# Optimization experiments

Hardware: AMD Instinct MI355X
Metric: run time of the kernel (lower is better)

Reference implementation:

```python
import jax, jax.numpy as jnp
import numpy as np

N, E, D, H, DK, T, R, KN, KR = 50000, 800000, 128, 8, 16, 3, 4, 2, 2

def setup_inputs() -> dict:
    key = jax.random.key(0)
    ks = jax.random.split(key, 16)
    lin_s = np.sqrt(1.0 / D).astype(np.float32)   # ~ nn.Linear init scale
    glo_s = np.sqrt(2.0 / (DK + DK)).astype(np.float32)  # glorot for [*,H,DK,DK]
    return {
        'x': jax.random.normal(ks[0], (N, D), jnp.float32),
        'Wk': jax.random.normal(ks[1], (KN, D, D), jnp.float32) * lin_s,
        'bk': jnp.zeros((KN, D), jnp.float32),
        'Wq': jax.random.normal(ks[2], (KN, D, D), jnp.float32) * lin_s,
        'bq': jnp.zeros((KN, D), jnp.float32),
        'Wv': jax.random.normal(ks[3], (KN, D, D), jnp.float32) * lin_s,
        'bv': jnp.zeros((KN, D), jnp.float32),
        'rel_pri': jnp.ones((KR, H), jnp.float32),
        'rel_att': jax.random.normal(ks[4], (KR, H, DK, DK), jnp.float32) * glo_s,
        'rel_msg': jax.random.normal(ks[5], (KR, H, DK, DK), jnp.float32) * glo_s,
        'n_alpha': jax.random.normal(ks[6], (T, KN), jnp.float32) * 0.001,
        'r_alpha': jax.random.normal(ks[7], (R, KR), jnp.float32) * 0.001,
        'W_up': jax.random.normal(ks[8], (T, D, D), jnp.float32) * lin_s,
        'b_up': jnp.zeros((T, D), jnp.float32),
        'gamma': jnp.ones((T, D), jnp.float32),
        'beta': jnp.zeros((T, D), jnp.float32),
        'edge_index': jax.random.randint(ks[9], (2, E), 0, N),
        'node_type': jax.random.randint(ks[10], (N,), 0, T),
        'edge_type': jax.random.randint(ks[11], (E,), 0, R),
    }

def reference(x, Wk, bk, Wq, bq, Wv, bv, rel_pri, rel_att, rel_msg,
              n_alpha, r_alpha, W_up, b_up, gamma, beta,
              edge_index, node_type, edge_type):
    n, d = x.shape
    h = rel_att.shape[1]; dk = d // h
    n_types = W_up.shape[0]; n_rel = r_alpha.shape[0]
    # NAS-mixed per-node-type k/q/v linears
    an = jax.nn.softmax(n_alpha, axis=-1)[node_type]        # [N, KN]
    def mix(W, b):
        cand = jnp.einsum('nd,kdo->kno', x, W) + b[:, None, :]  # [KN, N, D]
        return jnp.einsum('kno,nk->no', cand, an).reshape(n, h, dk)
    k = mix(Wk, bk); q = mix(Wq, bq); v = mix(Wv, bv)
    # NAS-mixed per-relation bilinear att/msg and priority
    br = jax.nn.softmax(r_alpha, axis=-1)                   # [R, KR]
    att_r = jnp.einsum('rk,khde->rhde', br, rel_att)        # [R, H, DK, DK]
    msg_r = jnp.einsum('rk,khde->rhde', br, rel_msg)
    pri_r = br @ rel_pri                                    # [R, H]
    src, dst = edge_index[0], edge_index[1]
    k_e = k[src]; q_e = q[dst]; v_e = v[src]                # [E, H, DK]
    k_t = jnp.zeros_like(k_e); m_t = jnp.zeros_like(v_e)
    for r in range(n_rel):  # small fixed relation loop
        sel = (edge_type == r)[:, None, None]
        k_t = k_t + jnp.where(sel, jnp.einsum('ehd,hdo->eho', k_e, att_r[r]), 0.0)
        m_t = m_t + jnp.where(sel, jnp.einsum('ehd,hdo->eho', v_e, msg_r[r]), 0.0)
    score = (q_e * k_t).sum(-1) * pri_r[edge_type] / np.float32(np.sqrt(dk))  # [E, H]
    # segment softmax over destination nodes
    mx = jax.ops.segment_max(score, dst, num_segments=n)
    ex = jnp.exp(score - mx[dst])
    den = jax.ops.segment_sum(ex, dst, num_segments=n)
    w = ex / (den[dst] + 1e-16)                             # [E, H]
    out = jax.ops.segment_sum(m_t * w[..., None], dst, num_segments=n).reshape(n, d)
    # heterogeneous update: gelu -> per-type linear -> residual -> per-type LN
    res = jax.nn.gelu(out)
    trans = jnp.zeros_like(x)
    for t in range(n_types):
        sel = (node_type == t)[:, None]
        trans = trans + jnp.where(sel, res @ W_up[t] + b_up[t], 0.0)
    hres = trans + x
    mu = hres.mean(-1, keepdims=True)
    var = hres.var(-1, keepdims=True)
    hn = (hres - mu) / jnp.sqrt(var + 1e-5)
    return hn * gamma[node_type] + beta[node_type]
```

## Files before the change

### kernel.cpp

```cpp
#include <hip/hip_runtime.h>
#include <hip/hip_bf16.h>

#define DEV __device__ __forceinline__

using frag8 = __attribute__((ext_vector_type(8))) short;
using f32x4 = __attribute__((ext_vector_type(4))) float;

DEV float b2f(__hip_bfloat16 v){ return __bfloat162float(v); }
DEV __hip_bfloat16 f2b(float f){ return __float2bfloat16(f); }
DEV short f2s(float f){ __hip_bfloat16 h = __float2bfloat16(f); short s; __builtin_memcpy(&s,&h,2); return s; }
DEV float bflo(unsigned u){ unsigned x = u<<16; float f; __builtin_memcpy(&f,&x,4); return f; }
DEV float bfhi(unsigned u){ unsigned x = u&0xFFFF0000u; float f; __builtin_memcpy(&f,&x,4); return f; }
DEV unsigned packbf(float a, float b){
  return (unsigned)(unsigned short)f2s(a) | ((unsigned)(unsigned short)f2s(b)<<16);
}

DEV bool is_bf16_mode(const void* rel_pri){
  return ((const unsigned*)rel_pri)[0] == 0x3F803F80u;
}
DEV float ldf(const void* p, int i, bool isbf){
  return isbf ? __bfloat162float(((const __hip_bfloat16*)p)[i]) : ((const float*)p)[i];
}

#if __has_builtin(__builtin_amdgcn_fdot2_f32_bf16)
typedef __bf16 bf16x2 __attribute__((ext_vector_type(2)));
DEV float dot2b(unsigned a, unsigned b, float c){
  bf16x2 av, bv; __builtin_memcpy(&av,&a,4); __builtin_memcpy(&bv,&b,4);
  return __builtin_amdgcn_fdot2_f32_bf16(av, bv, c, false);
}
#else
DEV float dot2b(unsigned a, unsigned b, float c){
  return c + bflo(a)*bflo(b) + bfhi(a)*bfhi(b);
}
#endif

DEV float gelu_f(float v){
  float z2 = v*(1.5957691216057308f + 0.07135481627f*v*v);
  return v/(1.f + __expf(-z2));
}

struct PrepArgs {
  const void *x,*Wk,*Wq,*Wv,*bk,*bq,*bv,*rel_pri,*rel_att,*rel_msg,*n_alpha,*r_alpha,*Wup,*bup,*gm,*bt;
  const int* ntype;
  float *anW,*priS,*bmixK,*bqt,*bvm,*upc;
  __hip_bfloat16 *bsw,*wsw,*msw2,*xb;
  int* count3;
  int N;
};

__global__ void k_prep(PrepArgs P){
  bool isbf = is_bf16_mode(P.rel_pri);
  float an[3][2], br[4][2];
  #pragma unroll
  for (int t=0;t<3;t++){
    float a0=ldf(P.n_alpha,t*2,isbf), a1=ldf(P.n_alpha,t*2+1,isbf);
    float m=fmaxf(a0,a1); float e0=__expf(a0-m), e1=__expf(a1-m); float inv=1.f/(e0+e1);
    an[t][0]=e0*inv; an[t][1]=e1*inv;
  }
  #pragma unroll
  for (int r=0;r<4;r++){
    float a0=ldf(P.r_alpha,r*2,isbf), a1=ldf(P.r_alpha,r*2+1,isbf);
    float m=fmaxf(a0,a1); float e0=__expf(a0-m), e1=__expf(a1-m); float inv=1.f/(e0+e1);
    br[r][0]=e0*inv; br[r][1]=e1*inv;
  }
  int g = blockIdx.x*blockDim.x + threadIdx.x;
  int stride = gridDim.x*blockDim.x;

  if (!isbf){
    const float4* xf = (const float4*)P.x;
    for (int idx=g; idx<P.N*16; idx+=stride){
      float4 u = xf[(size_t)idx*2], v = xf[(size_t)idx*2+1];
      frag8 r;
      r[0]=f2s(u.x); r[1]=f2s(u.y); r[2]=f2s(u.z); r[3]=f2s(u.w);
      r[4]=f2s(v.x); r[5]=f2s(v.y); r[6]=f2s(v.z); r[7]=f2s(v.w);
      *reinterpret_cast<frag8*>(P.xb + (size_t)idx*8) = r;
    }
  }

  for (int idx=g; idx<196608; idx+=stride){
    int jj = idx&7, lane=(idx>>3)&63, s=(idx>>9)&3, tile=(idx>>11)&15, chunk=idx>>15;
    int k = s*32 + ((lane>>4)<<3) + jj;
    int col = tile*16 + (lane&15);
    int cand = col>>7, c = col&127;
    float v;
    if (chunk==0)      v = ldf(P.Wk, cand*16384 + k*128 + c, isbf);
    else if (chunk==1) v = ldf(P.Wv, cand*16384 + k*128 + c, isbf);
    else {
      int r = chunk-2, h = c>>4, d = c&15;
      float acc=0.f;
      #pragma unroll
      for (int o=0;o<16;o++){
        float att = br[r][0]*ldf(P.rel_att,(h*16+d)*16+o,isbf) + br[r][1]*ldf(P.rel_att,2048+(h*16+d)*16+o,isbf);
        acc += ldf(P.Wq, cand*16384 + k*128 + h*16+o, isbf) * att;
      }
      v = acc;
    }
    P.bsw[idx] = f2b(v);
  }
  for (int idx=g; idx<49152; idx+=stride){
    int t3 = idx>>14, f = idx&16383;
    int jj=f&7, lane=(f>>3)&63, s=(f>>9)&3, nt=f>>11;
    int k = s*32 + ((lane>>4)<<3)+jj;
    int cc = nt*16 + (lane&15);
    P.wsw[idx] = f2b(ldf(P.Wup, t3*16384 + k*128 + cc, isbf));
  }
  for (int idx=g; idx<65536; idx+=stride){
    int rel = idx>>14, f = idx&16383;
    int jj=f&7, lane=(f>>3)&63, s=(f>>9)&3, tile=(f>>11)&7;
    int k = s*32 + ((lane>>4)<<3)+jj;
    int col = tile*16 + (lane&15);
    int h = k>>4, d = k&15;
    int h2 = col>>4, o = col&15;
    float v = 0.f;
    if (h2==h)
      v = br[rel][0]*ldf(P.rel_msg,(h*16+d)*16+o,isbf) + br[rel][1]*ldf(P.rel_msg,2048+(h*16+d)*16+o,isbf);
    P.msw2[idx] = f2b(v);
  }
  for (int idx=g; idx<384; idx+=stride){
    int t = idx>>7, c = idx&127;
    P.bmixK[idx] = an[t][0]*ldf(P.bk,c,isbf) + an[t][1]*ldf(P.bk,128+c,isbf);
  }
  for (int idx=g; idx<1536; idx+=stride){
    int t = idx>>9, rem = idx&511, r = rem>>7, c = rem&127;
    int h = c>>4, d = c&15;
    float acc=0.f;
    #pragma unroll
    for (int o=0;o<16;o++){
      float att = br[r][0]*ldf(P.rel_att,(h*16+d)*16+o,isbf) + br[r][1]*ldf(P.rel_att,2048+(h*16+d)*16+o,isbf);
      float bqm = an[t][0]*ldf(P.bq,h*16+o,isbf) + an[t][1]*ldf(P.bq,128+h*16+o,isbf);
      acc += bqm*att;
    }
    P.bqt[idx] = acc;
  }
  for (int idx=g; idx<384; idx+=stride){
    int t = idx>>7, c = idx&127;
    P.bvm[idx] = an[t][0]*ldf(P.bv,c,isbf) + an[t][1]*ldf(P.bv,128+c,isbf);
  }
  for (int idx=g; idx<1152; idx+=stride){
    int p = idx/384, rem = idx - p*384;
    const void* src = p==0 ? P.bup : p==1 ? P.gm : P.bt;
    P.upc[idx] = ldf(src, rem, isbf);
  }
  for (int idx=g; idx<32; idx+=stride){
    int r = idx>>3, h = idx&7;
    P.priS[idx] = 0.25f*(br[r][0]*ldf(P.rel_pri,h,isbf) + br[r][1]*ldf(P.rel_pri,8+h,isbf));
  }
  for (int idx=g; idx<6; idx+=stride) P.anW[idx] = an[idx>>1][idx&1];
  {
    int c0=0, c1=0, c2=0;
    for (int idx=g; idx<P.N; idx+=stride){
      int t = P.ntype[idx];
      c0 += (t==0); c1 += (t==1); c2 += (t==2);
    }
    #pragma unroll
    for (int m=1; m<64; m<<=1){
      c0 += __shfl_xor(c0, m, 64);
      c1 += __shfl_xor(c1, m, 64);
      c2 += __shfl_xor(c2, m, 64);
    }
    if ((threadIdx.x & 63) == 0){
      if (c0) atomicAdd(&P.count3[0], c0);
      if (c1) atomicAdd(&P.count3[1], c1);
      if (c2) atomicAdd(&P.count3[2], c2);
    }
  }
}

__global__ void k_hist(const int* __restrict__ eidx, int* __restrict__ count, int E){
  int e = blockIdx.x*256 + threadIdx.x;
  if (e < E) atomicAdd(&count[eidx[E+e]], 1);
}

__global__ __launch_bounds__(1024) void k_scan1(const int* __restrict__ count, int* __restrict__ excl,
                                                int* __restrict__ ctot, int N){
  __shared__ int s[1024];
  int i = blockIdx.x*1024 + threadIdx.x;
  int v = (i < N) ? count[i] : 0;
  s[threadIdx.x] = v;
  __syncthreads();
  int run = v;
  for (int off=1; off<1024; off<<=1){
    int add = (threadIdx.x >= off) ? s[threadIdx.x - off] : 0;
    __syncthreads();
    run += add; s[threadIdx.x] = run;
    __syncthreads();
  }
  if (i < N) excl[i] = run - v;
  if (threadIdx.x == 1023) ctot[blockIdx.x] = run;
}

__global__ void k_scan2(const int* __restrict__ ctot, int* __restrict__ coff,
                        const int* __restrict__ c3, int* __restrict__ segp, int NC){
  if (threadIdx.x==0 && blockIdx.x==0){
    int run=0;
    for (int c=0;c<NC;c++){ coff[c]=run; run+=ctot[c]; }
    int a0 = (c3[0]+127)&~127;
    int a1 = (c3[1]+127)&~127;
    int a2 = (c3[2]+127)&~127;
    segp[0]=0; segp[1]=a0; segp[2]=a0+a1; segp[3]=a0+a1+a2;
  }
}

__global__ __launch_bounds__(256) void k_nscatter(const int* __restrict__ ntype, const int* __restrict__ segp,
                           int* __restrict__ cur3, int* __restrict__ nlist, int N){
  __shared__ int wcnt[4][3];
  __shared__ int tbase[3];
  int tid = threadIdx.x;
  int n = blockIdx.x*256 + tid;
  int w = tid>>6, lane = tid&63;
  int t = (n < N) ? ntype[n] : -1;
  unsigned long long b0 = __ballot(t==0);
  unsigned long long b1 = __ballot(t==1);
  unsigned long long b2 = __ballot(t==2);
  if (lane==0){
    wcnt[w][0] = __popcll(b0);
    wcnt[w][1] = __popcll(b1);
    wcnt[w][2] = __popcll(b2);
  }
  __syncthreads();
  if (tid < 3){
    int c = wcnt[0][tid]+wcnt[1][tid]+wcnt[2][tid]+wcnt[3][tid];
    tbase[tid] = c ? atomicAdd(&cur3[tid], c) : 0;
  }
  __syncthreads();
  if (t >= 0){
    unsigned long long mask = t==0?b0 : t==1?b1 : b2;
    int lanerank = __popcll(mask & ((1ULL<<lane)-1ULL));
    int waveoff = 0;
    #pragma unroll
    for (int ww=0; ww<4; ww++) if (ww < w) waveoff += wcnt[ww][t];
    nlist[segp[t] + tbase[t] + waveoff + lanerank] = n;
  }
}

__global__ void k_escatter(const int* __restrict__ eidx, const int* __restrict__ etype,
                           const int* __restrict__ coff, const int* __restrict__ excl,
                           int* __restrict__ cursor, int* __restrict__ pack, int E){
  int e = blockIdx.x*256 + threadIdx.x;
  if (e < E){
    int src = eidx[e];
    int dst = eidx[E+e];
    int rt  = etype[e];
    int pos = coff[dst>>10] + excl[dst] + atomicAdd(&cursor[dst], 1);
    pack[pos] = src | (rt<<20);
  }
}

__global__ __launch_bounds__(256) void k_qkvqt(
    const void* __restrict__ x, const __hip_bfloat16* __restrict__ xb,
    const int* __restrict__ ntype,
    const void* __restrict__ relp,
    const __hip_bfloat16* __restrict__ bsw, const float* __restrict__ anW,
    const float* __restrict__ bmixK, const float* __restrict__ bmixV,
    const float* __restrict__ bqt,
    __hip_bfloat16* __restrict__ kb, __hip_bfloat16* __restrict__ vb,
    __hip_bfloat16* __restrict__ qtb, int N, int perx)
{
  __shared__ __hip_bfloat16 Bs[16384];
  __shared__ __align__(16) __hip_bfloat16 Os[128*72];
  bool isbf = is_bf16_mode(relp);
  int tid = threadIdx.x;
  int w = tid>>6, lane = tid&63;
  int m16 = lane&15, q4 = lane>>4;

  int nrb = (N+127)>>7;
  int xcd  = blockIdx.x & 7;
  int slot = blockIdx.x >> 3;
  int lrb  = slot/12;
  int sub  = slot - lrb*12;
  int rb   = xcd*perx + lrb;
  if (rb >= nrb) return;
  int chunk = sub >> 1;
  int hh    = sub & 1;
  int base  = rb*128;

  const int4* bsw4 = reinterpret_cast<const int4*>(bsw) + chunk*4096;
  int4* Bs4 = reinterpret_cast<int4*>(Bs);
  #pragma unroll
  for (int u=0;u<8;u++){
    int srcT = 4*hh + (u&3) + ((u>>2)<<3);
    __builtin_amdgcn_global_load_lds(
        (const __attribute__((address_space(1))) void*)(bsw4 + srcT*256 + tid),
        (__attribute__((address_space(3))) void*)(Bs4 + u*256 + tid),
        16, 0, 0);
  }

  const __hip_bfloat16* xs = isbf ? (const __hip_bfloat16*)x : xb;
  frag8 a0[4], a1[4];
  {
    int rr0 = base + w*32 + m16;
    int rr1 = rr0 + 16;
    int r0 = rr0 < N ? rr0 : N-1;
    int r1 = rr1 < N ? rr1 : N-1;
    #pragma unroll
    for (int s=0;s<4;s++){
      a0[s] = *reinterpret_cast<const frag8*>(xs + (size_t)r0*128 + q4*8 + s*32);
      a1[s] = *reinterpret_cast<const frag8*>(xs + (size_t)r1*128 + q4*8 + s*32);
    }
  }
  float e0[8], e1[8]; int tt8[8];
  #pragma unroll
  for (int u=0;u<8;u++){
    int rs = u>>2, i = u&3;
    int rr = base + w*32 + rs*16 + q4*4 + i;
    int rc = rr < N ? rr : N-1;
    int t = ntype[rc]; tt8[u] = t;
    e0[u] = anW[t*2]; e1[u] = anW[t*2+1];
  }
  float b0p[4], b1p[4], b2p[4];
  #pragma unroll
  for (int p=0;p<4;p++){
    int c = (4*hh + p)*16 + m16;
    if (chunk < 2){
      const float* bb = (chunk==0) ? bmixK : bmixV;
      b0p[p] = bb[c]; b1p[p] = bb[128+c]; b2p[p] = bb[256+c];
    } else {
      int r = chunk-2;
      b0p[p] = bqt[(0*4+r)*128 + c];
      b1p[p] = bqt[(1*4+r)*128 + c];
      b2p[p] = bqt[(2*4+r)*128 + c];
    }
  }
  __syncthreads();
  const frag8* Bf = reinterpret_cast<const frag8*>(Bs);
  #pragma unroll
  for (int p=0;p<4;p++){
    f32x4 c00={0,0,0,0}, c01={0,0,0,0}, c10={0,0,0,0}, c11={0,0,0,0};
    #pragma unroll
    for (int s=0;s<4;s++){
      frag8 b0 = Bf[(p*4+s)*64 + lane];
      frag8 b1 = Bf[((p+4)*4+s)*64 + lane];
      c00 = __builtin_amdgcn_mfma_f32_16x16x32_bf16(a0[s], b0, c00, 0,0,0);
      c01 = __builtin_amdgcn_mfma_f32_16x16x32_bf16(a1[s], b0, c01, 0,0,0);
      c10 = __builtin_amdgcn_mfma_f32_16x16x32_bf16(a0[s], b1, c10, 0,0,0);
      c11 = __builtin_amdgcn_mfma_f32_16x16x32_bf16(a1[s], b1, c11, 0,0,0);
    }
    int cl = p*16 + m16;
    #pragma unroll
    for (int u=0;u<8;u++){
      int rs = u>>2, i = u&3;
      float v0 = rs ? c01[i] : c00[i];
      float v1 = rs ? c11[i] : c10[i];
      int t = tt8[u];
      float bs = (t==0) ? b0p[p] : (t==1) ? b1p[p] : b2p[p];
      float val = e0[u]*v0 + e1[u]*v1 + bs;
      int rl = w*32 + rs*16 + q4*4 + i;
      Os[rl*72 + cl] = f2b(val);
    }
  }
  __syncthreads();
  #pragma unroll
  for (int it=0; it<4; it++){
    int idx = it*256 + tid;
    int rl = idx>>3, sl = idx&7;
    int row = base + rl;
    if (row < N){
      int4 val = *reinterpret_cast<const int4*>(
          reinterpret_cast<const char*>(Os) + rl*144 + sl*16);
      if (chunk < 2)
        *reinterpret_cast<int4*>((chunk==0?kb:vb) + (size_t)row*128 + hh*64 + sl*8) = val;
      else
        *reinterpret_cast<int4*>(qtb + (size_t)row*512 + (chunk-2)*128 + hh*64 + sl*8) = val;
    }
  }
}

__global__ __launch_bounds__(256) void k_vmsg(
    const __hip_bfloat16* __restrict__ vb,
    const __hip_bfloat16* __restrict__ msw2,
    __hip_bfloat16* __restrict__ vmb, int N, int perx)
{
  __shared__ __hip_bfloat16 Bs[16384];
  __shared__ __align__(16) __hip_bfloat16 Os[128*72];
  int tid = threadIdx.x, w = tid>>6, lane = tid&63, m16 = lane&15, q4 = lane>>4;
  int nrb = (N+127)>>7;
  int xcd = blockIdx.x & 7, slot = blockIdx.x>>3;
  int lrb = slot>>3, sub = slot&7;
  int rel = sub>>1, hh = sub&1;
  int rb = xcd*perx + lrb;
  if (rb >= nrb) return;
  int base = rb*128;

  const int4* m4 = reinterpret_cast<const int4*>(msw2) + rel*2048;
  int4* Bs4 = reinterpret_cast<int4*>(Bs);
  #pragma unroll
  for (int u=0;u<4;u++)
    __builtin_amdgcn_global_load_lds(
        (const __attribute__((address_space(1))) void*)(m4 + (4*hh+u)*256 + tid),
        (__attribute__((address_space(3))) void*)(Bs4 + u*256 + tid), 16, 0, 0);

  frag8 a0[4], a1[4];
  int rr0 = base + w*32 + m16, rr1 = rr0+16;
  int r0 = rr0<N?rr0:N-1, r1 = rr1<N?rr1:N-1;
  #pragma unroll
  for (int s=0;s<4;s++){
    a0[s] = *reinterpret_cast<const frag8*>(vb + (size_t)r0*128 + q4*8 + s*32);
    a1[s] = *reinterpret_cast<const frag8*>(vb + (size_t)r1*128 + q4*8 + s*32);
  }
  __syncthreads();
  const frag8* Bf = reinterpret_cast<const frag8*>(Bs);
  #pragma unroll
  for (int p=0;p<4;p++){
    f32x4 c0={0,0,0,0}, c1={0,0,0,0};
    #pragma unroll
    for (int s=0;s<4;s++){
      frag8 b = Bf[(p*4+s)*64 + lane];
      c0 = __builtin_amdgcn_mfma_f32_16x16x32_bf16(a0[s], b, c0, 0,0,0);
      c1 = __builtin_amdgcn_mfma_f32_16x16x32_bf16(a1[s], b, c1, 0,0,0);
    }
    int cl = p*16 + m16;
    #pragma unroll
    for (int u=0;u<8;u++){
      int rs = u>>2, i = u&3;
      float v = rs ? c1[i] : c0[i];
      int rl = w*32 + rs*16 + q4*4 + i;
      Os[rl*72 + cl] = f2b(v);
    }
  }
  __syncthreads();
  #pragma unroll
  for (int it=0; it<4; it++){
    int idx = it*256 + tid;
    int rl = idx>>3, sl = idx&7;
    int row = base + rl;
    if (row < N){
      int4 val = *reinterpret_cast<const int4*>(
          reinterpret_cast<const char*>(Os) + rl*144 + sl*16);
      *reinterpret_cast<int4*>(vmb + (size_t)row*512 + rel*128 + hh*64 + sl*8) = val;
    }
  }
}

__global__ __launch_bounds__(256) void k_aggr(
  const __hip_bfloat16* __restrict__ kb, const __hip_bfloat16* __restrict__ vmb,
  const __hip_bfloat16* __restrict__ qtb,
  const int* __restrict__ count, const int* __restrict__ excl, const int* __restrict__ coff,
  const int* __restrict__ pack, const float* __restrict__ priS,
  __hip_bfloat16* __restrict__ accb, float* __restrict__ denb, int N)
{
  __shared__ int4 Qs[4][64];
  int w = threadIdx.x>>6, lane = threadIdx.x&63;
  int n = blockIdx.x*4 + w; if (n >= N) return;
  int sub = lane&15, e4 = lane>>4;
  int h = sub>>1, half = sub&1;
  const char* kbB = (const char*)kb;
  const char* vmB = (const char*)vmb;
  int start = coff[n>>10] + excl[n];
  int deg = count[n];

  Qs[w][lane] = ((const int4*)qtb)[(size_t)n*64 + lane];
  float ps0 = priS[h], ps1 = priS[8+h], ps2 = priS[16+h], ps3 = priS[24+h];
  unsigned sub16 = (unsigned)sub<<4;

  float acc[8];
  #pragma unroll
  for (int d=0;d<8;d++) acc[d]=0.f;
  float den = 0.f;

  for (int b0=0; b0<deg; b0+=64){
    int m = deg - b0; if (m > 64) m = 64;
    int pk = (lane < m) ? pack[start + b0 + lane] : 0;
    int nst = (m + 3)>>2;
    int4 K={0,0,0,0}, V={0,0,0,0}; int RT=0; bool A=false;
    auto issue = [&](int st){
      int j = st*4 + e4;
      A = j < m;
      int pe = __shfl(pk, j, 64);
      RT = (pe>>20)&3;
      unsigned src = (unsigned)(pe & 0xFFFFF);
      if (A){
        K = *(const int4*)(kbB + ((src<<8) + sub16));
        V = *(const int4*)(vmB + ((src<<10) + ((unsigned)RT<<8) + sub16));
      } else {
        K = int4{0,0,0,0}; V = int4{0,0,0,0};
      }
    };
    issue(0);
    for (int st=0; st<nst; st++){
      int4 kc=K, vc=V; int rt=RT; bool a=A;
      if (st+1 < nst) issue(st+1);
      int4 qc = Qs[w][rt*16 + sub];
      float psr = rt==0 ? ps0 : rt==1 ? ps1 : rt==2 ? ps2 : ps3;
      float s = dot2b((unsigned)kc.x,(unsigned)qc.x,0.f);
      s = dot2b((unsigned)kc.y,(unsigned)qc.y,s);
      s = dot2b((unsigned)kc.z,(unsigned)qc.z,s);
      s = dot2b((unsigned)kc.w,(unsigned)qc.w,s);
      s += __shfl_xor(s, 1, 64);
      float ex = a ? __expf(fminf(s*psr, 30.f)) : 0.f;
      den += half ? 0.f : ex;
      unsigned vv[4]={(unsigned)vc.x,(unsigned)vc.y,(unsigned)vc.z,(unsigned)vc.w};
      #pragma unroll
      for (int q=0;q<4;q++){
        acc[2*q]   += ex*bflo(vv[q]);
        acc[2*q+1] += ex*bfhi(vv[q]);
      }
    }
  }
  #pragma unroll
  for (int m2=16; m2<64; m2<<=1){
    #pragma unroll
    for (int d=0;d<8;d++) acc[d] += __shfl_xor(acc[d], m2, 64);
    den += __shfl_xor(den, m2, 64);
  }
  if (e4==0){
    unsigned o0 = packbf(acc[0], acc[1]);
    unsigned o1 = packbf(acc[2], acc[3]);
    unsigned o2 = packbf(acc[4], acc[5]);
    unsigned o3 = packbf(acc[6], acc[7]);
    int4 o4; o4.x=(int)o0; o4.y=(int)o1; o4.z=(int)o2; o4.w=(int)o3;
    ((int4*)accb)[(size_t)n*16 + sub] = o4;
    if (half==0) denb[(size_t)n*8 + h] = den;
  }
}

__global__ __launch_bounds__(256) void k_msgup(
  const __hip_bfloat16* __restrict__ accb, const float* __restrict__ denb,
  const void* __restrict__ x, const void* __restrict__ relp,
  const int* __restrict__ nlist, const int* __restrict__ segp,
  const __hip_bfloat16* __restrict__ wsw,
  const float* __restrict__ upc, void* __restrict__ out, int N)
{
  __shared__ __hip_bfloat16 Ms[16384];
  __shared__ __hip_bfloat16 resS[64*136];
  __shared__ int nrow[64];
  bool isbf = is_bf16_mode(relp);
  int tid=threadIdx.x, w=tid>>6, lane=tid&63, m16=lane&15, q4=lane>>4;
  int pos0 = blockIdx.x*64;
  int sg1 = segp[1], sg2 = segp[2];
  int t = (pos0 >= sg2) ? 2 : (pos0 >= sg1) ? 1 : 0;
  if (tid < 64) nrow[tid] = nlist[pos0 + tid];
  const int4* wsw4 = reinterpret_cast<const int4*>(wsw) + t*2048;
  int4* Ms4 = reinterpret_cast<int4*>(Ms);
  #pragma unroll
  for (int u=0;u<8;u++)
    __builtin_amdgcn_global_load_lds(
        (const __attribute__((address_space(1))) void*)(wsw4 + u*256 + tid),
        (__attribute__((address_space(3))) void*)(Ms4 + u*256 + tid), 16, 0, 0);
  __syncthreads();

  int nC[4]; float xr[4][8];
  #pragma unroll
  for (int u=0;u<4;u++){
    int rr = w*16 + q4*4 + u;
    int nid = nrow[rr]; nC[u] = nid;
    int nc = nid<0?0:nid;
    #pragma unroll
    for (int nt=0;nt<8;nt++){
      int col = nt*16+m16;
      xr[u][nt] = isbf ? b2f(((const __hip_bfloat16*)x)[(size_t)nc*128+col])
                       : ((const float*)x)[(size_t)nc*128+col];
    }
  }

  const int4* acc4 = (const int4*)accb;
  #pragma unroll
  for (int it=0; it<4; it++){
    int t2 = it*256 + tid;
    int row = t2>>4, seg = t2&15;
    int nid = nrow[row]; int nc = nid<0?0:nid;
    int4 a = acc4[(size_t)nc*16 + seg];
    float rdn = 1.f/(denb[(size_t)nc*8 + (seg>>1)] + 1e-16f);
    unsigned uu[4] = {(unsigned)a.x,(unsigned)a.y,(unsigned)a.z,(unsigned)a.w};
    unsigned ov[4];
    #pragma unroll
    for (int q=0;q<4;q++){
      float v0 = bflo(uu[q])*rdn, v1 = bfhi(uu[q])*rdn;
      ov[q] = packbf(gelu_f(v0), gelu_f(v1));
    }
    int4 o4; o4.x=(int)ov[0]; o4.y=(int)ov[1]; o4.z=(int)ov[2]; o4.w=(int)ov[3];
    *reinterpret_cast<int4*>(reinterpret_cast<char*>(resS) + row*272 + seg*16) = o4;
  }
  __syncthreads();

  f32x4 d[8];
  #pragma unroll
  for (int nt=0;nt<8;nt++) d[nt]={0,0,0,0};
  const frag8* Bf2 = reinterpret_cast<const frag8*>(Ms);
  #pragma unroll
  for (int s=0;s<4;s++){
    frag8 a = *reinterpret_cast<const frag8*>(&resS[(w*16 + m16)*136 + s*32 + q4*8]);
    #pragma unroll
    for (int nt=0;nt<8;nt++){
      frag8 b = Bf2[(nt*4+s)*64 + lane];
      d[nt] = __builtin_amdgcn_mfma_f32_16x16x32_bf16(a, b, d[nt], 0,0,0);
    }
  }
  #pragma unroll
  for (int u=0;u<4;u++){
    int nid = nC[u];
    float hv[8], s1=0.f, s2=0.f;
    #pragma unroll
    for (int nt=0;nt<8;nt++){
      int col = nt*16+m16;
      float v = d[nt][u] + upc[t*128+col] + xr[u][nt];
      hv[nt]=v; s1+=v; s2+=v*v;
    }
    #pragma unroll
    for (int mm=1; mm<16; mm<<=1){ s1 += __shfl_xor(s1, mm, 16); s2 += __shfl_xor(s2, mm, 16); }
    float mu = s1*(1.f/128.f);
    float var = s2*(1.f/128.f) - mu*mu;
    float rcp = rsqrtf(var + 1e-5f);
    if (nid >= 0){
      #pragma unroll
      for (int nt=0;nt<8;nt++){
        int col = nt*16+m16;
        float o = (hv[nt]-mu)*rcp*upc[384 + t*128+col] + upc[768 + t*128+col];
        if (isbf) ((__hip_bfloat16*)out)[(size_t)nid*128+col] = f2b(o);
        else      ((float*)out)[(size_t)nid*128+col] = o;
      }
    }
  }
}

extern "C" void kernel_launch(void* const* d_in, const int* in_sizes, int n_in,
                              void* d_out, int out_size, void* d_ws, size_t ws_size,
                              hipStream_t stream)
{
  const int* eidx  = (const int*)d_in[16];
  const int* ntype = (const int*)d_in[17];
  const int* etype = (const int*)d_in[18];

  const int N  = in_sizes[0]/128;
  const int E  = in_sizes[18];
  const int NC = (N + 1023)/1024;

  char* ws = (char*)d_ws;
  size_t off = 0;
  auto alloc = [&](size_t bytes){ size_t o = off; off += (bytes + 255) & ~(size_t)255; return o; };
  size_t o_count = alloc((size_t)N*4);
  size_t o_cursor= alloc((size_t)N*4);
  size_t o_c3    = alloc(16);
  size_t o_cur3  = alloc(16);
  size_t zbytes  = off;
  size_t o_nlist = alloc((size_t)(N+1024)*4);
  size_t o_excl  = alloc((size_t)N*4);
  size_t o_ctot  = alloc(256);
  size_t o_coff  = alloc(256);
  size_t o_segp  = alloc(16);
  size_t o_an    = alloc(6*4);
  size_t o_pri   = alloc(32*4);
  size_t o_bmk   = alloc(384*4);
  size_t o_bmv   = alloc(384*4);
  size_t o_bqt   = alloc(1536*4);
  size_t o_upc   = alloc(1152*4);
  size_t o_bsw   = alloc(196608*2);
  size_t o_wsw   = alloc(49152*2);
  size_t o_msw   = alloc(65536*2);
  size_t o_pack  = alloc((size_t)E*4);
  size_t o_xb    = alloc((size_t)N*128*2);
  size_t o_kb    = alloc((size_t)N*128*2);
  size_t o_vb    = alloc((size_t)N*128*2);
  size_t o_qt    = alloc((size_t)N*512*2);
  size_t o_vm    = alloc((size_t)N*512*2);
  size_t o_acc   = alloc((size_t)N*128*2);
  size_t o_den   = alloc((size_t)N*8*4);
  (void)ws_size; (void)n_in; (void)out_size;

  hipMemsetAsync(ws, 0, zbytes, stream);
  hipMemsetAsync(ws + o_nlist, 0xFF, (size_t)(N+1024)*4, stream);

  PrepArgs P;
  P.x=d_in[0];
  P.Wk=d_in[1]; P.bk=d_in[2]; P.Wq=d_in[3]; P.bq=d_in[4]; P.Wv=d_in[5]; P.bv=d_in[6];
  P.rel_pri=d_in[7]; P.rel_att=d_in[8]; P.rel_msg=d_in[9];
  P.n_alpha=d_in[10]; P.r_alpha=d_in[11]; P.Wup=d_in[12]; P.bup=d_in[13]; P.gm=d_in[14]; P.bt=d_in[15];
  P.ntype=ntype;
  P.anW=(float*)(ws+o_an); P.priS=(float*)(ws+o_pri);
  P.bmixK=(float*)(ws+o_bmk); P.bqt=(float*)(ws+o_bqt); P.bvm=(float*)(ws+o_bmv);
  P.upc=(float*)(ws+o_upc);
  P.bsw=(__hip_bfloat16*)(ws+o_bsw); P.wsw=(__hip_bfloat16*)(ws+o_wsw);
  P.msw2=(__hip_bfloat16*)(ws+o_msw);
  P.xb=(__hip_bfloat16*)(ws+o_xb);
  P.count3=(int*)(ws+o_c3); P.N=N;
  k_prep<<<1024, 256, 0, stream>>>(P);

  k_hist<<<(E+255)/256, 256, 0, stream>>>(eidx, (int*)(ws+o_count), E);
  k_scan1<<<NC, 1024, 0, stream>>>((const int*)(ws+o_count), (int*)(ws+o_excl), (int*)(ws+o_ctot), N);
  k_scan2<<<1, 64, 0, stream>>>((const int*)(ws+o_ctot), (int*)(ws+o_coff),
                                (const int*)(ws+o_c3), (int*)(ws+o_segp), NC);
  k_nscatter<<<(N+255)/256, 256, 0, stream>>>(ntype, (const int*)(ws+o_segp),
                                              (int*)(ws+o_cur3), (int*)(ws+o_nlist), N);
  k_escatter<<<(E+255)/256, 256, 0, stream>>>(eidx, etype, (const int*)(ws+o_coff),
                                              (const int*)(ws+o_excl), (int*)(ws+o_cursor),
                                              (int*)(ws+o_pack), E);
  int nrb  = (N + 127)/128;
  int perx = (nrb + 7)/8;
  k_qkvqt<<<perx*12*8, 256, 0, stream>>>(d_in[0], (const __hip_bfloat16*)(ws+o_xb), ntype, d_in[7],
                                           (const __hip_bfloat16*)(ws+o_bsw),
                                           (const float*)(ws+o_an), (const float*)(ws+o_bmk),
                                           (const float*)(ws+o_bmv),
                                           (const float*)(ws+o_bqt),
                                           (__hip_bfloat16*)(ws+o_kb), (__hip_bfloat16*)(ws+o_vb),
                                           (__hip_bfloat16*)(ws+o_qt), N, perx);
  k_vmsg<<<perx*8*8, 256, 0, stream>>>((const __hip_bfloat16*)(ws+o_vb),
                                       (const __hip_bfloat16*)(ws+o_msw),
                                       (__hip_bfloat16*)(ws+o_vm), N, perx);
  k_aggr<<<(N+3)/4, 256, 0, stream>>>((const __hip_bfloat16*)(ws+o_kb), (const __hip_bfloat16*)(ws+o_vm),
                                (const __hip_bfloat16*)(ws+o_qt),
                                (const int*)(ws+o_count), (const int*)(ws+o_excl),
                                (const int*)(ws+o_coff), (const int*)(ws+o_pack),
                                (const float*)(ws+o_pri),
                                (__hip_bfloat16*)(ws+o_acc), (float*)(ws+o_den), N);
  int gUp = (N + 444)/64;
  k_msgup<<<gUp, 256, 0, stream>>>((const __hip_bfloat16*)(ws+o_acc), (const float*)(ws+o_den),
                                   d_in[0], d_in[7],
                                   (const int*)(ws+o_nlist), (const int*)(ws+o_segp),
                                   (const __hip_bfloat16*)(ws+o_wsw),
                                   (const float*)(ws+o_upc), d_out, N);
}
```

Measured before the change: 397.2 us.

## Apply relation message transform after aggregation instead of precomputing per-relation V

Removes the k_vmsg kernel that materialized V·msg for all four relations per node. The aggregation kernel now gathers raw V and keeps four per-relation accumulators, writing a 4x wider acc buffer. The msg matrices are then applied once per destination node by an MFMA in k_msgup, before normalization and GELU. This trades a large intermediate write/read and heavier gathers for more registers in k_aggr, divergent per-relation branches, and a larger acc buffer.

```diff
diff --git a/kernel.cpp b/kernel.cpp
--- a/kernel.cpp
+++ b/kernel.cpp
@@ -104,16 +104,13 @@
     int cc = nt*16 + (lane&15);
     P.wsw[idx] = f2b(ldf(P.Wup, t3*16384 + k*128 + cc, isbf));
   }
-  for (int idx=g; idx<65536; idx+=stride){
-    int rel = idx>>14, f = idx&16383;
-    int jj=f&7, lane=(f>>3)&63, s=(f>>9)&3, tile=(f>>11)&7;
-    int k = s*32 + ((lane>>4)<<3)+jj;
-    int col = tile*16 + (lane&15);
-    int h = k>>4, d = k&15;
-    int h2 = col>>4, o = col&15;
-    float v = 0.f;
-    if (h2==h)
-      v = br[rel][0]*ldf(P.rel_msg,(h*16+d)*16+o,isbf) + br[rel][1]*ldf(P.rel_msg,2048+(h*16+d)*16+o,isbf);
+  for (int idx=g; idx<8192; idx+=stride){
+    int jj=idx&7, lane=(idx>>3)&63, s=(idx>>9)&1, h=idx>>10;
+    int k64 = s*32 + ((lane>>4)<<3) + jj;
+    int rel = k64>>4, d = k64&15;
+    int o = lane&15;
+    float v = br[rel][0]*ldf(P.rel_msg,(h*16+d)*16+o,isbf)
+            + br[rel][1]*ldf(P.rel_msg,2048+(h*16+d)*16+o,isbf);
     P.msw2[idx] = f2b(v);
   }
   for (int idx=g; idx<384; idx+=stride){
@@ -365,74 +362,8 @@
   }
 }
 
-__global__ __launch_bounds__(256) void k_vmsg(
-    const __hip_bfloat16* __restrict__ vb,
-    const __hip_bfloat16* __restrict__ msw2,
-    __hip_bfloat16* __restrict__ vmb, int N, int perx)
-{
-  __shared__ __hip_bfloat16 Bs[16384];
-  __shared__ __align__(16) __hip_bfloat16 Os[128*72];
-  int tid = threadIdx.x, w = tid>>6, lane = tid&63, m16 = lane&15, q4 = lane>>4;
-  int nrb = (N+127)>>7;
-  int xcd = blockIdx.x & 7, slot = blockIdx.x>>3;
-  int lrb = slot>>3, sub = slot&7;
-  int rel = sub>>1, hh = sub&1;
-  int rb = xcd*perx + lrb;
-  if (rb >= nrb) return;
-  int base = rb*128;
-
-  const int4* m4 = reinterpret_cast<const int4*>(msw2) + rel*2048;
-  int4* Bs4 = reinterpret_cast<int4*>(Bs);
-  #pragma unroll
-  for (int u=0;u<4;u++)
-    __builtin_amdgcn_global_load_lds(
-        (const __attribute__((address_space(1))) void*)(m4 + (4*hh+u)*256 + tid),
-        (__attribute__((address_space(3))) void*)(Bs4 + u*256 + tid), 16, 0, 0);
-
-  frag8 a0[4], a1[4];
-  int rr0 = base + w*32 + m16, rr1 = rr0+16;
-  int r0 = rr0<N?rr0:N-1, r1 = rr1<N?rr1:N-1;
-  #pragma unroll
-  for (int s=0;s<4;s++){
-    a0[s] = *reinterpret_cast<const frag8*>(vb + (size_t)r0*128 + q4*8 + s*32);
-    a1[s] = *reinterpret_cast<const frag8*>(vb + (size_t)r1*128 + q4*8 + s*32);
-  }
-  __syncthreads();
-  const frag8* Bf = reinterpret_cast<const frag8*>(Bs);
-  #pragma unroll
-  for (int p=0;p<4;p++){
-    f32x4 c0={0,0,0,0}, c1={0,0,0,0};
-    #pragma unroll
-    for (int s=0;s<4;s++){
-      frag8 b = Bf[(p*4+s)*64 + lane];
-      c0 = __builtin_amdgcn_mfma_f32_16x16x32_bf16(a0[s], b, c0, 0,0,0);
-      c1 = __builtin_amdgcn_mfma_f32_16x16x32_bf16(a1[s], b, c1, 0,0,0);
-    }
-    int cl = p*16 + m16;
-    #pragma unroll
-    for (int u=0;u<8;u++){
-      int rs = u>>2, i = u&3;
-      float v = rs ? c1[i] : c0[i];
-      int rl = w*32 + rs*16 + q4*4 + i;
-      Os[rl*72 + cl] = f2b(v);
-    }
-  }
-  __syncthreads();
-  #pragma unroll
-  for (int it=0; it<4; it++){
-    int idx = it*256 + tid;
-    int rl = idx>>3, sl = idx&7;
-    int row = base + rl;
-    if (row < N){
-      int4 val = *reinterpret_cast<const int4*>(
-          reinterpret_cast<const char*>(Os) + rl*144 + sl*16);
-      *reinterpret_cast<int4*>(vmb + (size_t)row*512 + rel*128 + hh*64 + sl*8) = val;
-    }
-  }
-}
-
 __global__ __launch_bounds__(256) void k_aggr(
-  const __hip_bfloat16* __restrict__ kb, const __hip_bfloat16* __restrict__ vmb,
+  const __hip_bfloat16* __restrict__ kb, const __hip_bfloat16* __restrict__ vb,
   const __hip_bfloat16* __restrict__ qtb,
   const int* __restrict__ count, const int* __restrict__ excl, const int* __restrict__ coff,
   const int* __restrict__ pack, const float* __restrict__ priS,
@@ -444,7 +375,7 @@
   int sub = lane&15, e4 = lane>>4;
   int h = sub>>1, half = sub&1;
   const char* kbB = (const char*)kb;
-  const char* vmB = (const char*)vmb;
+  const char* vbB = (const char*)vb;
   int start = coff[n>>10] + excl[n];
   int deg = count[n];
 
@@ -452,9 +383,9 @@
   float ps0 = priS[h], ps1 = priS[8+h], ps2 = priS[16+h], ps3 = priS[24+h];
   unsigned sub16 = (unsigned)sub<<4;
 
-  float acc[8];
-  #pragma unroll
-  for (int d=0;d<8;d++) acc[d]=0.f;
+  float a0_[8], a1_[8], a2_[8], a3_[8];
+  #pragma unroll
+  for (int d=0;d<8;d++){ a0_[d]=0.f; a1_[d]=0.f; a2_[d]=0.f; a3_[d]=0.f; }
   float den = 0.f;
 
   for (int b0=0; b0<deg; b0+=64){
@@ -470,7 +401,7 @@
       unsigned src = (unsigned)(pe & 0xFFFFF);
       if (A){
         K = *(const int4*)(kbB + ((src<<8) + sub16));
-        V = *(const int4*)(vmB + ((src<<10) + ((unsigned)RT<<8) + sub16));
+        V = *(const int4*)(vbB + ((src<<8) + sub16));
       } else {
         K = int4{0,0,0,0}; V = int4{0,0,0,0};
       }
@@ -489,26 +420,47 @@
       float ex = a ? __expf(fminf(s*psr, 30.f)) : 0.f;
       den += half ? 0.f : ex;
       unsigned vv[4]={(unsigned)vc.x,(unsigned)vc.y,(unsigned)vc.z,(unsigned)vc.w};
-      #pragma unroll
-      for (int q=0;q<4;q++){
-        acc[2*q]   += ex*bflo(vv[q]);
-        acc[2*q+1] += ex*bfhi(vv[q]);
+      if (rt==0){
+        #pragma unroll
+        for (int q=0;q<4;q++){ a0_[2*q] += ex*bflo(vv[q]); a0_[2*q+1] += ex*bfhi(vv[q]); }
+      } else if (rt==1){
+        #pragma unroll
+        for (int q=0;q<4;q++){ a1_[2*q] += ex*bflo(vv[q]); a1_[2*q+1] += ex*bfhi(vv[q]); }
+      } else if (rt==2){
+        #pragma unroll
+        for (int q=0;q<4;q++){ a2_[2*q] += ex*bflo(vv[q]); a2_[2*q+1] += ex*bfhi(vv[q]); }
+      } else {
+        #pragma unroll
+        for (int q=0;q<4;q++){ a3_[2*q] += ex*bflo(vv[q]); a3_[2*q+1] += ex*bfhi(vv[q]); }
       }
     }
   }
   #pragma unroll
   for (int m2=16; m2<64; m2<<=1){
     #pragma unroll
-    for (int d=0;d<8;d++) acc[d] += __shfl_xor(acc[d], m2, 64);
+    for (int d=0;d<8;d++){
+      a0_[d] += __shfl_xor(a0_[d], m2, 64);
+      a1_[d] += __shfl_xor(a1_[d], m2, 64);
+      a2_[d] += __shfl_xor(a2_[d], m2, 64);
+      a3_[d] += __shfl_xor(a3_[d], m2, 64);
+    }
     den += __shfl_xor(den, m2, 64);
   }
   if (e4==0){
-    unsigned o0 = packbf(acc[0], acc[1]);
-    unsigned o1 = packbf(acc[2], acc[3]);
-    unsigned o2 = packbf(acc[4], acc[5]);
-    unsigned o3 = packbf(acc[6], acc[7]);
-    int4 o4; o4.x=(int)o0; o4.y=(int)o1; o4.z=(int)o2; o4.w=(int)o3;
-    ((int4*)accb)[(size_t)n*16 + sub] = o4;
+    char* ab = (char*)accb + (size_t)n*1024 + h*128 + half*16;
+    int4 o;
+    o.x=(int)packbf(a0_[0],a0_[1]); o.y=(int)packbf(a0_[2],a0_[3]);
+    o.z=(int)packbf(a0_[4],a0_[5]); o.w=(int)packbf(a0_[6],a0_[7]);
+    *reinterpret_cast<int4*>(ab) = o;
+    o.x=(int)packbf(a1_[0],a1_[1]); o.y=(int)packbf(a1_[2],a1_[3]);
+    o.z=(int)packbf(a1_[4],a1_[5]); o.w=(int)packbf(a1_[6],a1_[7]);
+    *reinterpret_cast<int4*>(ab + 32) = o;
+    o.x=(int)packbf(a2_[0],a2_[1]); o.y=(int)packbf(a2_[2],a2_[3]);
+    o.z=(int)packbf(a2_[4],a2_[5]); o.w=(int)packbf(a2_[6],a2_[7]);
+    *reinterpret_cast<int4*>(ab + 64) = o;
+    o.x=(int)packbf(a3_[0],a3_[1]); o.y=(int)packbf(a3_[2],a3_[3]);
+    o.z=(int)packbf(a3_[4],a3_[5]); o.w=(int)packbf(a3_[6],a3_[7]);
+    *reinterpret_cast<int4*>(ab + 96) = o;
     if (half==0) denb[(size_t)n*8 + h] = den;
   }
 }
@@ -517,7 +469,7 @@
   const __hip_bfloat16* __restrict__ accb, const float* __restrict__ denb,
   const void* __restrict__ x, const void* __restrict__ relp,
   const int* __restrict__ nlist, const int* __restrict__ segp,
-  const __hip_bfloat16* __restrict__ wsw,
+  const __hip_bfloat16* __restrict__ mswB, const __hip_bfloat16* __restrict__ wsw,
   const float* __restrict__ upc, void* __restrict__ out, int N)
 {
   __shared__ __hip_bfloat16 Ms[16384];
@@ -529,47 +481,62 @@
   int sg1 = segp[1], sg2 = segp[2];
   int t = (pos0 >= sg2) ? 2 : (pos0 >= sg1) ? 1 : 0;
   if (tid < 64) nrow[tid] = nlist[pos0 + tid];
+  int4* Ms4 = reinterpret_cast<int4*>(Ms);
+  const int4* mb4 = reinterpret_cast<const int4*>(mswB);
+  #pragma unroll
+  for (int u=0;u<4;u++)
+    __builtin_amdgcn_global_load_lds(
+        (const __attribute__((address_space(1))) void*)(mb4 + u*256 + tid),
+        (__attribute__((address_space(3))) void*)(Ms4 + u*256 + tid), 16, 0, 0);
+  __syncthreads();
+
+  int nA = nrow[w*16 + m16]; int nAc = nA < 0 ? 0 : nA;
+  int nC[4];
+  #pragma unroll
+  for (int u=0;u<4;u++) nC[u] = nrow[w*16 + q4*4 + u];
+
+  float xr[4][8];
+  #pragma unroll
+  for (int u=0;u<4;u++){
+    int nid = nC[u]; int nc = nid<0?0:nid;
+    #pragma unroll
+    for (int nt=0;nt<8;nt++){
+      int col = nt*16+m16;
+      xr[u][nt] = isbf ? b2f(((const __hip_bfloat16*)x)[(size_t)nc*128+col])
+                       : ((const float*)x)[(size_t)nc*128+col];
+    }
+  }
+
+  const frag8* Bf = reinterpret_cast<const frag8*>(Ms);
+  f32x4 dm[8];
+  #pragma unroll
+  for (int h=0;h<8;h++) dm[h] = f32x4{0,0,0,0};
+  #pragma unroll
+  for (int h=0;h<8;h++){
+    #pragma unroll
+    for (int s=0;s<2;s++){
+      frag8 a = *reinterpret_cast<const frag8*>(accb + (size_t)nAc*512 + h*64 + s*32 + q4*8);
+      dm[h] = __builtin_amdgcn_mfma_f32_16x16x32_bf16(a, Bf[(h*2+s)*64 + lane], dm[h], 0,0,0);
+    }
+  }
+  #pragma unroll
+  for (int u=0;u<4;u++){
+    int nid = nC[u]; int nc = nid<0?0:nid;
+    int rr = w*16 + q4*4 + u;
+    #pragma unroll
+    for (int h=0;h<8;h++){
+      float dn = denb[(size_t)nc*8 + h];
+      float vv = dm[h][u] / (dn + 1e-16f);
+      resS[rr*136 + h*16 + m16] = f2b(gelu_f(vv));
+    }
+  }
+  __syncthreads();
   const int4* wsw4 = reinterpret_cast<const int4*>(wsw) + t*2048;
-  int4* Ms4 = reinterpret_cast<int4*>(Ms);
   #pragma unroll
   for (int u=0;u<8;u++)
     __builtin_amdgcn_global_load_lds(
         (const __attribute__((address_space(1))) void*)(wsw4 + u*256 + tid),
         (__attribute__((address_space(3))) void*)(Ms4 + u*256 + tid), 16, 0, 0);
-  __syncthreads();
-
-  int nC[4]; float xr[4][8];
-  #pragma unroll
-  for (int u=0;u<4;u++){
-    int rr = w*16 + q4*4 + u;
-    int nid = nrow[rr]; nC[u] = nid;
-    int nc = nid<0?0:nid;
-    #pragma unroll
-    for (int nt=0;nt<8;nt++){
-      int col = nt*16+m16;
-      xr[u][nt] = isbf ? b2f(((const __hip_bfloat16*)x)[(size_t)nc*128+col])
-                       : ((const float*)x)[(size_t)nc*128+col];
-    }
-  }
-
-  const int4* acc4 = (const int4*)accb;
-  #pragma unroll
-  for (int it=0; it<4; it++){
-    int t2 = it*256 + tid;
-    int row = t2>>4, seg = t2&15;
-    int nid = nrow[row]; int nc = nid<0?0:nid;
-    int4 a = acc4[(size_t)nc*16 + seg];
-    float rdn = 1.f/(denb[(size_t)nc*8 + (seg>>1)] + 1e-16f);
-    unsigned uu[4] = {(unsigned)a.x,(unsigned)a.y,(unsigned)a.z,(unsigned)a.w};
-    unsigned ov[4];
-    #pragma unroll
-    for (int q=0;q<4;q++){
-      float v0 = bflo(uu[q])*rdn, v1 = bfhi(uu[q])*rdn;
-      ov[q] = packbf(gelu_f(v0), gelu_f(v1));
-    }
-    int4 o4; o4.x=(int)ov[0]; o4.y=(int)ov[1]; o4.z=(int)ov[2]; o4.w=(int)ov[3];
-    *reinterpret_cast<int4*>(reinterpret_cast<char*>(resS) + row*272 + seg*16) = o4;
-  }
   __syncthreads();
 
   f32x4 d[8];
@@ -645,14 +612,13 @@
   size_t o_upc   = alloc(1152*4);
   size_t o_bsw   = alloc(196608*2);
   size_t o_wsw   = alloc(49152*2);
-  size_t o_msw   = alloc(65536*2);
+  size_t o_msw   = alloc(8192*2);
   size_t o_pack  = alloc((size_t)E*4);
   size_t o_xb    = alloc((size_t)N*128*2);
   size_t o_kb    = alloc((size_t)N*128*2);
   size_t o_vb    = alloc((size_t)N*128*2);
   size_t o_qt    = alloc((size_t)N*512*2);
-  size_t o_vm    = alloc((size_t)N*512*2);
-  size_t o_acc   = alloc((size_t)N*128*2);
+  size_t o_acc   = alloc((size_t)N*512*2);
   size_t o_den   = alloc((size_t)N*8*4);
   (void)ws_size; (void)n_in; (void)out_size;
 
@@ -692,10 +658,7 @@
                                            (const float*)(ws+o_bqt),
                                            (__hip_bfloat16*)(ws+o_kb), (__hip_bfloat16*)(ws+o_vb),
                                            (__hip_bfloat16*)(ws+o_qt), N, perx);
-  k_vmsg<<<perx*8*8, 256, 0, stream>>>((const __hip_bfloat16*)(ws+o_vb),
-                                       (const __hip_bfloat16*)(ws+o_msw),
-                                       (__hip_bfloat16*)(ws+o_vm), N, perx);
-  k_aggr<<<(N+3)/4, 256, 0, stream>>>((const __hip_bfloat16*)(ws+o_kb), (const __hip_bfloat16*)(ws+o_vm),
+  k_aggr<<<(N+3)/4, 256, 0, stream>>>((const __hip_bfloat16*)(ws+o_kb), (const __hip_bfloat16*)(ws+o_vb),
                                 (const __hip_bfloat16*)(ws+o_qt),
                                 (const int*)(ws+o_count), (const int*)(ws+o_excl),
                                 (const int*)(ws+o_coff), (const int*)(ws+o_pack),
@@ -705,6 +668,7 @@
   k_msgup<<<gUp, 256, 0, stream>>>((const __hip_bfloat16*)(ws+o_acc), (const float*)(ws+o_den),
                                    d_in[0], d_in[7],
                                    (const int*)(ws+o_nlist), (const int*)(ws+o_segp),
+                                   (const __hip_bfloat16*)(ws+o_msw),
                                    (const __hip_bfloat16*)(ws+o_wsw),
                                    (const float*)(ws+o_upc), d_out, N);
 }
```

Result: no change. 399.5 us (+0.6%).

## Merge prep/hist, scan stages, and scatter/QKV kernels into fewer launches

Applied to the files above, without the earlier changes.

Combines several small kernels into fewer launches. Prep and the edge histogram become one kernel split by block index. The two-stage scan becomes a single kernel where the last block, found through an atomic counter, computes the block offsets. Node scatter, edge scatter and the QKV GEMM also share one launch with block-range dispatch. The aim is to cut launch overhead and let independent work overlap across blocks, at the cost of a larger shared-memory footprint for the scatter blocks and reliance on a last-block fence pattern.

```diff
diff --git a/kernel.cpp b/kernel.cpp
--- a/kernel.cpp
+++ b/kernel.cpp
@@ -48,7 +48,7 @@
   int N;
 };
 
-__global__ void k_prep(PrepArgs P){
+DEV void prep_work(const PrepArgs& P, int g, int stride){
   bool isbf = is_bf16_mode(P.rel_pri);
   float an[3][2], br[4][2];
   #pragma unroll
@@ -63,8 +63,6 @@
     float m=fmaxf(a0,a1); float e0=__expf(a0-m), e1=__expf(a1-m); float inv=1.f/(e0+e1);
     br[r][0]=e0*inv; br[r][1]=e1*inv;
   }
-  int g = blockIdx.x*blockDim.x + threadIdx.x;
-  int stride = gridDim.x*blockDim.x;
 
   if (!isbf){
     const float4* xf = (const float4*)P.x;
@@ -105,15 +103,14 @@
     P.wsw[idx] = f2b(ldf(P.Wup, t3*16384 + k*128 + cc, isbf));
   }
   for (int idx=g; idx<65536; idx+=stride){
-    int rel = idx>>14, f = idx&16383;
-    int jj=f&7, lane=(f>>3)&63, s=(f>>9)&3, tile=(f>>11)&7;
+    int jj=idx&7, lane=(idx>>3)&63, s=(idx>>9)&3, tile=(idx>>11)&7, kc=idx>>14;
     int k = s*32 + ((lane>>4)<<3)+jj;
     int col = tile*16 + (lane&15);
     int h = k>>4, d = k&15;
     int h2 = col>>4, o = col&15;
     float v = 0.f;
     if (h2==h)
-      v = br[rel][0]*ldf(P.rel_msg,(h*16+d)*16+o,isbf) + br[rel][1]*ldf(P.rel_msg,2048+(h*16+d)*16+o,isbf);
+      v = br[kc][0]*ldf(P.rel_msg,(h*16+d)*16+o,isbf) + br[kc][1]*ldf(P.rel_msg,2048+(h*16+d)*16+o,isbf);
     P.msw2[idx] = f2b(v);
   }
   for (int idx=g; idx<384; idx+=stride){
@@ -166,14 +163,22 @@
   }
 }
 
-__global__ void k_hist(const int* __restrict__ eidx, int* __restrict__ count, int E){
-  int e = blockIdx.x*256 + threadIdx.x;
-  if (e < E) atomicAdd(&count[eidx[E+e]], 1);
-}
-
-__global__ __launch_bounds__(1024) void k_scan1(const int* __restrict__ count, int* __restrict__ excl,
-                                                int* __restrict__ ctot, int N){
+__global__ __launch_bounds__(256) void k_fuse1(PrepArgs P, const int* __restrict__ eidx,
+                                               int* __restrict__ count, int E, int prepBlocks){
+  if ((int)blockIdx.x < prepBlocks){
+    prep_work(P, blockIdx.x*256 + threadIdx.x, prepBlocks*256);
+  } else {
+    int e = (blockIdx.x - prepBlocks)*256 + threadIdx.x;
+    if (e < E) atomicAdd(&count[eidx[E+e]], 1);
+  }
+}
+
+__global__ __launch_bounds__(1024) void k_scan(const int* __restrict__ count, int* __restrict__ excl,
+                                               int* __restrict__ ctot, int* __restrict__ coff,
+                                               const int* __restrict__ c3, int* __restrict__ segp,
+                                               int* __restrict__ done, int N, int NC){
   __shared__ int s[1024];
+  __shared__ int amLast;
   int i = blockIdx.x*1024 + threadIdx.x;
   int v = (i < N) ? count[i] : 0;
   s[threadIdx.x] = v;
@@ -186,14 +191,15 @@
     __syncthreads();
   }
   if (i < N) excl[i] = run - v;
-  if (threadIdx.x == 1023) ctot[blockIdx.x] = run;
-}
-
-__global__ void k_scan2(const int* __restrict__ ctot, int* __restrict__ coff,
-                        const int* __restrict__ c3, int* __restrict__ segp, int NC){
-  if (threadIdx.x==0 && blockIdx.x==0){
-    int run=0;
-    for (int c=0;c<NC;c++){ coff[c]=run; run+=ctot[c]; }
+  if (threadIdx.x == 1023){
+    ctot[blockIdx.x] = run;
+    __threadfence();
+    amLast = (atomicAdd(done, 1) == (int)gridDim.x - 1);
+  }
+  __syncthreads();
+  if (amLast && threadIdx.x == 0){
+    int run2 = 0;
+    for (int c=0;c<NC;c++){ coff[c]=run2; run2 += atomicAdd(&ctot[c],0); }
     int a0 = (c3[0]+127)&~127;
     int a1 = (c3[1]+127)&~127;
     int a2 = (c3[2]+127)&~127;
@@ -201,71 +207,77 @@
   }
 }
 
-__global__ __launch_bounds__(256) void k_nscatter(const int* __restrict__ ntype, const int* __restrict__ segp,
-                           int* __restrict__ cur3, int* __restrict__ nlist, int N){
-  __shared__ int wcnt[4][3];
-  __shared__ int tbase[3];
-  int tid = threadIdx.x;
-  int n = blockIdx.x*256 + tid;
-  int w = tid>>6, lane = tid&63;
-  int t = (n < N) ? ntype[n] : -1;
-  unsigned long long b0 = __ballot(t==0);
-  unsigned long long b1 = __ballot(t==1);
-  unsigned long long b2 = __ballot(t==2);
-  if (lane==0){
-    wcnt[w][0] = __popcll(b0);
-    wcnt[w][1] = __popcll(b1);
-    wcnt[w][2] = __popcll(b2);
-  }
-  __syncthreads();
-  if (tid < 3){
-    int c = wcnt[0][tid]+wcnt[1][tid]+wcnt[2][tid]+wcnt[3][tid];
-    tbase[tid] = c ? atomicAdd(&cur3[tid], c) : 0;
-  }
-  __syncthreads();
-  if (t >= 0){
-    unsigned long long mask = t==0?b0 : t==1?b1 : b2;
-    int lanerank = __popcll(mask & ((1ULL<<lane)-1ULL));
-    int waveoff = 0;
-    #pragma unroll
-    for (int ww=0; ww<4; ww++) if (ww < w) waveoff += wcnt[ww][t];
-    nlist[segp[t] + tbase[t] + waveoff + lanerank] = n;
-  }
-}
-
-__global__ void k_escatter(const int* __restrict__ eidx, const int* __restrict__ etype,
-                           const int* __restrict__ coff, const int* __restrict__ excl,
-                           int* __restrict__ cursor, int* __restrict__ pack, int E){
-  int e = blockIdx.x*256 + threadIdx.x;
-  if (e < E){
-    int src = eidx[e];
-    int dst = eidx[E+e];
-    int rt  = etype[e];
-    int pos = coff[dst>>10] + excl[dst] + atomicAdd(&cursor[dst], 1);
-    pack[pos] = src | (rt<<20);
-  }
-}
-
-__global__ __launch_bounds__(256) void k_qkvqt(
+__global__ __launch_bounds__(256) void k_fuse4(
+    const int* __restrict__ ntype, const int* __restrict__ segp,
+    int* __restrict__ cur3, int* __restrict__ nlist,
+    const int* __restrict__ eidx, const int* __restrict__ etype,
+    const int* __restrict__ coff, const int* __restrict__ excl,
+    int* __restrict__ cursor, int* __restrict__ pack,
     const void* __restrict__ x, const __hip_bfloat16* __restrict__ xb,
-    const int* __restrict__ ntype,
     const void* __restrict__ relp,
     const __hip_bfloat16* __restrict__ bsw, const float* __restrict__ anW,
     const float* __restrict__ bmixK, const float* __restrict__ bmixV,
     const float* __restrict__ bqt,
     __hip_bfloat16* __restrict__ kb, __hip_bfloat16* __restrict__ vb,
-    __hip_bfloat16* __restrict__ qtb, int N, int perx)
+    __hip_bfloat16* __restrict__ qtb,
+    int N, int E, int perx, int gNs, int gEs)
 {
-  __shared__ __hip_bfloat16 Bs[16384];
-  __shared__ __align__(16) __hip_bfloat16 Os[128*72];
+  __shared__ __align__(16) char smem[51200];
+  int tid = threadIdx.x;
+  int bid = blockIdx.x;
+
+  if (bid < gNs){
+    int* wcnt  = (int*)smem;
+    int* tbase = (int*)(smem + 48);
+    int n = bid*256 + tid;
+    int w = tid>>6, lane = tid&63;
+    int t = (n < N) ? ntype[n] : -1;
+    unsigned long long b0 = __ballot(t==0);
+    unsigned long long b1 = __ballot(t==1);
+    unsigned long long b2 = __ballot(t==2);
+    if (lane==0){
+      wcnt[w*3+0] = __popcll(b0);
+      wcnt[w*3+1] = __popcll(b1);
+      wcnt[w*3+2] = __popcll(b2);
+    }
+    __syncthreads();
+    if (tid < 3){
+      int c = wcnt[0*3+tid]+wcnt[1*3+tid]+wcnt[2*3+tid]+wcnt[3*3+tid];
+      tbase[tid] = c ? atomicAdd(&cur3[tid], c) : 0;
+    }
+    __syncthreads();
+    if (t >= 0){
+      unsigned long long mask = t==0?b0 : t==1?b1 : b2;
+      int lanerank = __popcll(mask & ((1ULL<<lane)-1ULL));
+      int waveoff = 0;
+      #pragma unroll
+      for (int ww=0; ww<4; ww++) if (ww < w) waveoff += wcnt[ww*3+t];
+      nlist[segp[t] + tbase[t] + waveoff + lanerank] = n;
+    }
+    return;
+  }
+  if (bid < gNs + gEs){
+    int e = (bid - gNs)*256 + tid;
+    if (e < E){
+      int src = eidx[e];
+      int dst = eidx[E+e];
+      int rt  = etype[e];
+      int pos = coff[dst>>10] + excl[dst] + atomicAdd(&cursor[dst], 1);
+      pack[pos] = src | (rt<<20);
+    }
+    return;
+  }
+
+  __hip_bfloat16* Bs = (__hip_bfloat16*)smem;
+  __hip_bfloat16* Os = (__hip_bfloat16*)(smem + 32768);
   bool isbf = is_bf16_mode(relp);
-  int tid = threadIdx.x;
   int w = tid>>6, lane = tid&63;
   int m16 = lane&15, q4 = lane>>4;
 
+  int bq = bid - gNs - gEs;
   int nrb = (N+127)>>7;
-  int xcd  = blockIdx.x & 7;
-  int slot = blockIdx.x >> 3;
+  int xcd  = bq & 7;
+  int slot = bq >> 3;
   int lrb  = slot/12;
   int sub  = slot - lrb*12;
   int rb   = xcd*perx + lrb;
@@ -631,6 +643,7 @@
   size_t o_cursor= alloc((size_t)N*4);
   size_t o_c3    = alloc(16);
   size_t o_cur3  = alloc(16);
+  size_t o_done  = alloc(16);
   size_t zbytes  = off;
   size_t o_nlist = alloc((size_t)(N+1024)*4);
   size_t o_excl  = alloc((size_t)N*4);
@@ -672,26 +685,28 @@
   P.msw2=(__hip_bfloat16*)(ws+o_msw);
   P.xb=(__hip_bfloat16*)(ws+o_xb);
   P.count3=(int*)(ws+o_c3); P.N=N;
-  k_prep<<<1024, 256, 0, stream>>>(P);
-
-  k_hist<<<(E+255)/256, 256, 0, stream>>>(eidx, (int*)(ws+o_count), E);
-  k_scan1<<<NC, 1024, 0, stream>>>((const int*)(ws+o_count), (int*)(ws+o_excl), (int*)(ws+o_ctot), N);
-  k_scan2<<<1, 64, 0, stream>>>((const int*)(ws+o_ctot), (int*)(ws+o_coff),
-                                (const int*)(ws+o_c3), (int*)(ws+o_segp), NC);
-  k_nscatter<<<(N+255)/256, 256, 0, stream>>>(ntype, (const int*)(ws+o_segp),
-                                              (int*)(ws+o_cur3), (int*)(ws+o_nlist), N);
-  k_escatter<<<(E+255)/256, 256, 0, stream>>>(eidx, etype, (const int*)(ws+o_coff),
-                                              (const int*)(ws+o_excl), (int*)(ws+o_cursor),
-                                              (int*)(ws+o_pack), E);
+
+  int gEh = (E+255)/256;
+  k_fuse1<<<1024 + gEh, 256, 0, stream>>>(P, eidx, (int*)(ws+o_count), E, 1024);
+
+  k_scan<<<NC, 1024, 0, stream>>>((const int*)(ws+o_count), (int*)(ws+o_excl),
+                                  (int*)(ws+o_ctot), (int*)(ws+o_coff),
+                                  (const int*)(ws+o_c3), (int*)(ws+o_segp),
+                                  (int*)(ws+o_done), N, NC);
+
   int nrb  = (N + 127)/128;
   int perx = (nrb + 7)/8;
-  k_qkvqt<<<perx*12*8, 256, 0, stream>>>(d_in[0], (const __hip_bfloat16*)(ws+o_xb), ntype, d_in[7],
-                                           (const __hip_bfloat16*)(ws+o_bsw),
-                                           (const float*)(ws+o_an), (const float*)(ws+o_bmk),
-                                           (const float*)(ws+o_bmv),
-                                           (const float*)(ws+o_bqt),
-                                           (__hip_bfloat16*)(ws+o_kb), (__hip_bfloat16*)(ws+o_vb),
-                                           (__hip_bfloat16*)(ws+o_qt), N, perx);
+  int gNs = (N+255)/256, gEs = (E+255)/256, gQ = perx*12*8;
+  k_fuse4<<<gNs+gEs+gQ, 256, 0, stream>>>(
+      ntype, (const int*)(ws+o_segp), (int*)(ws+o_cur3), (int*)(ws+o_nlist),
+      eidx, etype, (const int*)(ws+o_coff), (const int*)(ws+o_excl),
+      (int*)(ws+o_cursor), (int*)(ws+o_pack),
+      d_in[0], (const __hip_bfloat16*)(ws+o_xb), d_in[7],
+      (const __hip_bfloat16*)(ws+o_bsw), (const float*)(ws+o_an),
+      (const float*)(ws+o_bmk), (const float*)(ws+o_bmv), (const float*)(ws+o_bqt),
+      (__hip_bfloat16*)(ws+o_kb), (__hip_bfloat16*)(ws+o_vb), (__hip_bfloat16*)(ws+o_qt),
+      N, E, perx, gNs, gEs);
+
   k_vmsg<<<perx*8*8, 256, 0, stream>>>((const __hip_bfloat16*)(ws+o_vb),
                                        (const __hip_bfloat16*)(ws+o_msw),
                                        (__hip_bfloat16*)(ws+o_vm), N, perx);
```

Result: faster. 370.6 us (-6.7%).
